# Performance work log

Hardware: AMD Instinct MI355X
Metric: run time of the kernel (lower is better)

Reference implementation:

```python
import jax, jax.numpy as jnp
import numpy as np

D_MODEL = 1024
NUM_HEADS = 16
D_K = D_MODEL // NUM_HEADS


def setup_inputs() -> dict:
    key = jax.random.key(0)
    ks = jax.random.split(key, 12)
    B, S, D = 4, 2048, D_MODEL
    s = 1.0 / np.sqrt(D)
    return {
        "q": jax.random.normal(ks[0], (B, S, D), jnp.float32),
        "k": jax.random.normal(ks[1], (B, S, D), jnp.float32),
        "v": jax.random.normal(ks[2], (B, S, D), jnp.float32),
        "w_q": jax.random.normal(ks[3], (D, D), jnp.float32) * s,
        "b_q": jax.random.normal(ks[4], (D,), jnp.float32) * s,
        "w_k": jax.random.normal(ks[5], (D, D), jnp.float32) * s,
        "b_k": jax.random.normal(ks[6], (D,), jnp.float32) * s,
        "w_v": jax.random.normal(ks[7], (D, D), jnp.float32) * s,
        "b_v": jax.random.normal(ks[8], (D,), jnp.float32) * s,
        "w_0": jax.random.normal(ks[9], (D, D), jnp.float32) * s,
        "b_0": jax.random.normal(ks[10], (D,), jnp.float32) * s,
    }


def reference(q, k, v, w_q, b_q, w_k, b_k, w_v, b_v, w_0, b_0):
    B = q.shape[0]
    H, dk = NUM_HEADS, D_K
    # project and split heads: [B,S,D] -> [B,H,S,dk]
    def split_heads(x):
        return x.reshape(B, -1, H, dk).transpose(0, 2, 1, 3)
    qh = split_heads(q @ w_q + b_q)
    kh = split_heads(k @ w_k + b_k)
    vh = split_heads(v @ w_v + b_v)
    scores = jnp.einsum("bhsd,bhtd->bhst", qh, kh) / np.sqrt(dk).astype(jnp.float32)
    dists = jax.nn.softmax(scores, axis=-1)
    attn = jnp.einsum("bhst,bhtd->bhsd", dists, vh)  # [B,H,S,dk]
    # NOTE: original torch code reshapes WITHOUT transposing heads back
    # (.contiguous().view(B, -1, d_model) on [B,H,S,dk]) -- reproduce faithfully.
    attn = attn.reshape(B, -1, D_MODEL)  # [B,S,D] with head-major interleave
    return attn @ w_0 + b_0
```

## Files before the change

kernel.cpp:

```cpp
#include <hip/hip_runtime.h>
#include <stdint.h>

typedef __bf16 bf16x8 __attribute__((ext_vector_type(8)));
typedef float  f32x4  __attribute__((ext_vector_type(4)));

union U16x8 { uint4 u; uint16_t s[8]; };

__device__ __forceinline__ uint16_t f2b(float f) {
    union { float f; uint32_t u; } c; c.f = f;
    uint32_t u = c.u;
    uint32_t r = u + 0x7fffu + ((u >> 16) & 1u);
    return (uint16_t)(r >> 16);
}

__device__ __forceinline__ uint32_t asu(float f) {
    union { float f; uint32_t u; } c; c.f = f; return c.u;
}
__device__ __forceinline__ uint32_t pack_bf16_hu(float a, float b) {
    uint32_t ua = asu(a) + 0x8000u, ub = asu(b) + 0x8000u;
    return (ua >> 16) | (ub & 0xffff0000u);
}

__device__ __forceinline__ void gl_lds16(const uint16_t* g, uint16_t* l) {
    __builtin_amdgcn_global_load_lds(
        (const __attribute__((address_space(1))) void*)g,
        (__attribute__((address_space(3))) void*)l, 16, 0, 0);
}

__global__ void cast3_f32_bf16(const float* __restrict__ x0, const float* __restrict__ x1,
                               const float* __restrict__ x2,
                               uint16_t* __restrict__ y0, uint16_t* __restrict__ y1,
                               uint16_t* __restrict__ y2, int n4) {
    const float* x; uint16_t* y;
    switch (blockIdx.y) {
        case 0: x = x0; y = y0; break;
        case 1: x = x1; y = y1; break;
        default: x = x2; y = y2; break;
    }
    int i = blockIdx.x * blockDim.x + threadIdx.x;
    if (i < n4) {
        float4 v = ((const float4*)x)[i];
        ushort4 o;
        o.x = f2b(v.x); o.y = f2b(v.y); o.z = f2b(v.z); o.w = f2b(v.w);
        *(ushort4*)(y + (size_t)i * 4) = o;
    }
}

__global__ void transpose_cast4(const float* __restrict__ W0, const float* __restrict__ W1,
                                const float* __restrict__ W2, const float* __restrict__ W3,
                                uint16_t* __restrict__ O0, uint16_t* __restrict__ O1,
                                uint16_t* __restrict__ O2, uint16_t* __restrict__ O3) {
    __shared__ float tile[64][65];
    const float* W; uint16_t* Wt;
    switch (blockIdx.z) {
        case 0: W = W0; Wt = O0; break;
        case 1: W = W1; Wt = O1; break;
        case 2: W = W2; Wt = O2; break;
        default: W = W3; Wt = O3; break;
    }
    const int k0 = blockIdx.y * 64, n0 = blockIdx.x * 64;
    const int tx = threadIdx.x & 63, ty = threadIdx.x >> 6;
    #pragma unroll
    for (int r = ty; r < 64; r += 4)
        tile[r][tx] = W[(size_t)(k0 + r) * 1024 + n0 + tx];
    __syncthreads();
    #pragma unroll
    for (int r = ty; r < 64; r += 4)
        Wt[(size_t)(n0 + r) * 1024 + k0 + tx] = f2b(tile[tx][r]);
}

__global__ __launch_bounds__(256, 3)
void gemm_qkv(const uint16_t* __restrict__ A0, const uint16_t* __restrict__ A1,
              const uint16_t* __restrict__ A2,
              const uint16_t* __restrict__ B0, const uint16_t* __restrict__ B1,
              const uint16_t* __restrict__ B2,
              const float* __restrict__ c0, const float* __restrict__ c1,
              const float* __restrict__ c2,
              uint16_t* __restrict__ O0, uint16_t* __restrict__ O1,
              uint16_t* __restrict__ O2, float qscale) {
    __shared__ uint16_t SH[2 * 128 * 32] __attribute__((aligned(16)));
    uint16_t* As = SH;
    uint16_t* Bs = SH + 128 * 32;

    const uint16_t* A; const uint16_t* Bt; const float* bias; uint16_t* Cout; float scale;
    switch (blockIdx.z) {
        case 0: A = A0; Bt = B0; bias = c0; Cout = O0; scale = qscale; break;
        case 1: A = A1; Bt = B1; bias = c1; Cout = O1; scale = 1.0f;  break;
        default: A = A2; Bt = B2; bias = c2; Cout = O2; scale = 1.0f; break;
    }

    const int tid = threadIdx.x;
    const int m0 = blockIdx.y * 128, n0 = blockIdx.x * 128;
    const int l = tid & 63, ln = l & 15, qd = l >> 4;
    const int w = tid >> 6;
    const int wm = (w >> 1) * 64, wn = (w & 1) * 64;

    f32x4 acc[4][4] = {};

    for (int kk = 0; kk < 1024; kk += 32) {
        __syncthreads();
        #pragma unroll
        for (int i = 0; i < 2; i++) {
            int c = tid + i * 256;
            gl_lds16(&A[(size_t)(m0 + (c >> 2)) * 1024 + kk + (c & 3) * 8], &As[c * 8]);
            gl_lds16(&Bt[(size_t)(n0 + (c >> 2)) * 1024 + kk + (c & 3) * 8], &Bs[c * 8]);
        }
        __syncthreads();

        bf16x8 af[4], bfr[4];
        #pragma unroll
        for (int i = 0; i < 4; i++)
            af[i] = *(const bf16x8*)&As[(wm + i * 16 + ln) * 32 + qd * 8];
        #pragma unroll
        for (int j = 0; j < 4; j++)
            bfr[j] = *(const bf16x8*)&Bs[(wn + j * 16 + ln) * 32 + qd * 8];
        #pragma unroll
        for (int i = 0; i < 4; i++)
            #pragma unroll
            for (int j = 0; j < 4; j++)
                acc[i][j] = __builtin_amdgcn_mfma_f32_16x16x32_bf16(af[i], bfr[j], acc[i][j], 0, 0, 0);
    }

    float bv[4];
    #pragma unroll
    for (int j = 0; j < 4; j++) bv[j] = bias[n0 + wn + j * 16 + ln];

    __syncthreads();
    uint16_t* scr = (uint16_t*)SH + w * 1024;
    const int colb = n0 + wn;
    const int h = colb >> 6;
    #pragma unroll
    for (int i = 0; i < 4; i++) {
        #pragma unroll
        for (int j = 0; j < 4; j++)
            #pragma unroll
            for (int r = 0; r < 4; r++)
                scr[(qd * 4 + r) * 64 + j * 16 + ln] = f2b((acc[i][j][r] + bv[j]) * scale);
        #pragma unroll
        for (int ii = 0; ii < 2; ii++) {
            int ch = ii * 64 + l, row = ch >> 3, sg = ch & 7;
            int grow = m0 + wm + i * 16 + row;
            int b = grow >> 11, s = grow & 2047;
            *(uint4*)&Cout[(size_t)((b * 16 + h) * 2048 + s) * 64 + sg * 8] =
                *(uint4*)&scr[row * 64 + sg * 8];
        }
    }
}

__global__ __launch_bounds__(256, 3)
void gemm_o(const uint16_t* __restrict__ A, const uint16_t* __restrict__ Bt,
            const float* __restrict__ bias, float* __restrict__ Cout) {
    __shared__ uint16_t SH[2 * 128 * 32] __attribute__((aligned(16)));
    uint16_t* As = SH;
    uint16_t* Bs = SH + 128 * 32;

    const int tid = threadIdx.x;
    const int m0 = blockIdx.y * 128, n0 = blockIdx.x * 128;
    const int l = tid & 63, ln = l & 15, qd = l >> 4;
    const int w = tid >> 6;
    const int wm = (w >> 1) * 64, wn = (w & 1) * 64;

    f32x4 acc[4][4] = {};

    for (int kk = 0; kk < 1024; kk += 32) {
        __syncthreads();
        #pragma unroll
        for (int i = 0; i < 2; i++) {
            int c = tid + i * 256;
            gl_lds16(&A[(size_t)(m0 + (c >> 2)) * 1024 + kk + (c & 3) * 8], &As[c * 8]);
            gl_lds16(&Bt[(size_t)(n0 + (c >> 2)) * 1024 + kk + (c & 3) * 8], &Bs[c * 8]);
        }
        __syncthreads();

        bf16x8 af[4], bfr[4];
        #pragma unroll
        for (int i = 0; i < 4; i++)
            af[i] = *(const bf16x8*)&As[(wm + i * 16 + ln) * 32 + qd * 8];
        #pragma unroll
        for (int j = 0; j < 4; j++)
            bfr[j] = *(const bf16x8*)&Bs[(wn + j * 16 + ln) * 32 + qd * 8];
        #pragma unroll
        for (int i = 0; i < 4; i++)
            #pragma unroll
            for (int j = 0; j < 4; j++)
                acc[i][j] = __builtin_amdgcn_mfma_f32_16x16x32_bf16(af[i], bfr[j], acc[i][j], 0, 0, 0);
    }

    float bv[4];
    #pragma unroll
    for (int j = 0; j < 4; j++) bv[j] = bias[n0 + wn + j * 16 + ln];

    __syncthreads();
    float* scr = (float*)SH + w * 1024;
    #pragma unroll
    for (int i = 0; i < 4; i++) {
        #pragma unroll
        for (int j = 0; j < 4; j++)
            #pragma unroll
            for (int r = 0; r < 4; r++)
                scr[(qd * 4 + r) * 64 + j * 16 + ln] = acc[i][j][r] + bv[j];
        #pragma unroll
        for (int ii = 0; ii < 4; ii++) {
            int ch = ii * 64 + l, row = ch >> 4, sg = ch & 15;
            *(float4*)&Cout[(size_t)(m0 + wm + i * 16 + row) * 1024 + n0 + wn + sg * 4] =
                *(float4*)&scr[row * 64 + sg * 4];
        }
    }
}

__global__ __launch_bounds__(512, 4)
void attn_kernel(const uint16_t* __restrict__ Qh, const uint16_t* __restrict__ Kh,
                 const uint16_t* __restrict__ Vh, uint16_t* __restrict__ Of) {
    __shared__ uint16_t Ks[64 * 72]  __attribute__((aligned(16)));
    __shared__ uint16_t Vt[64 * 72]  __attribute__((aligned(16)));
    __shared__ uint16_t Ps[256 * 72] __attribute__((aligned(16)));

    const int tid = threadIdx.x;
    const int w = tid >> 6, l = tid & 63, ln = l & 15, qd = l >> 4;
    const size_t base = (size_t)blockIdx.y * 131072;
    const int q0 = blockIdx.x * 256;

    bf16x8 qf[2][2];
    #pragma unroll
    for (int tq = 0; tq < 2; tq++)
        #pragma unroll
        for (int ks = 0; ks < 2; ks++)
            qf[tq][ks] = *(const bf16x8*)&Qh[base + (size_t)(q0 + w * 32 + tq * 16 + ln) * 64 + ks * 32 + qd * 8];

    f32x4 oacc[2][4] = {};
    float mrun[2] = { -__builtin_inff(), -__builtin_inff() };
    float lrun[2] = { 0.f, 0.f };

    for (int j = 0; j < 32; j++) {
        const int t0 = j * 64;
        __syncthreads();
        if (w >= 4) {
            int idx = tid - 256;
            #pragma unroll
            for (int i = 0; i < 2; i++) {
                int c = idx + i * 256, tr = c >> 3, sg = c & 7;
                *(uint4*)&Ks[tr * 72 + sg * 8] =
                    *(const uint4*)&Kh[base + (size_t)(t0 + tr) * 64 + sg * 8];
            }
        } else {
            int u = tid & 31, sg = tid >> 5;
            U16x8 r0, r1;
            r0.u = *(const uint4*)&Vh[base + (size_t)(t0 + 2 * u) * 64 + sg * 8];
            r1.u = *(const uint4*)&Vh[base + (size_t)(t0 + 2 * u + 1) * 64 + sg * 8];
            #pragma unroll
            for (int e = 0; e < 8; e++) {
                uint32_t pk = (uint32_t)r0.s[e] | ((uint32_t)r1.s[e] << 16);
                *(uint32_t*)&Vt[(sg * 8 + e) * 72 + 2 * u] = pk;
            }
        }
        __syncthreads();

        bf16x8 kb[4][2];
        #pragma unroll
        for (int tt = 0; tt < 4; tt++)
            #pragma unroll
            for (int ks = 0; ks < 2; ks++)
                kb[tt][ks] = *(const bf16x8*)&Ks[(tt * 16 + ln) * 72 + ks * 32 + qd * 8];
        f32x4 sa[4][2] = {};
        #pragma unroll
        for (int tt = 0; tt < 4; tt++)
            #pragma unroll
            for (int tq = 0; tq < 2; tq++)
                #pragma unroll
                for (int ks = 0; ks < 2; ks++)
                    sa[tt][tq] = __builtin_amdgcn_mfma_f32_16x16x32_bf16(kb[tt][ks], qf[tq][ks], sa[tt][tq], 0, 0, 0);

        float alpha[2];
        #pragma unroll
        for (int tq = 0; tq < 2; tq++) {
            float mx = -__builtin_inff();
            #pragma unroll
            for (int tt = 0; tt < 4; tt++)
                #pragma unroll
                for (int r = 0; r < 4; r++) mx = fmaxf(mx, sa[tt][tq][r]);
            mx = fmaxf(mx, __shfl_xor(mx, 16));
            mx = fmaxf(mx, __shfl_xor(mx, 32));
            float mnew = fmaxf(mrun[tq], mx);
            alpha[tq] = __builtin_amdgcn_exp2f(mrun[tq] - mnew);
            mrun[tq] = mnew;
            float rs = 0.f;
            #pragma unroll
            for (int tt = 0; tt < 4; tt++)
                #pragma unroll
                for (int r = 0; r < 4; r++) {
                    float p = __builtin_amdgcn_exp2f(sa[tt][tq][r] - mnew);
                    sa[tt][tq][r] = p; rs += p;
                }
            rs += __shfl_xor(rs, 16);
            rs += __shfl_xor(rs, 32);
            lrun[tq] = lrun[tq] * alpha[tq] + rs;
            #pragma unroll
            for (int tt = 0; tt < 4; tt++) {
                uint2 pk;
                pk.x = pack_bf16_hu(sa[tt][tq][0], sa[tt][tq][1]);
                pk.y = pack_bf16_hu(sa[tt][tq][2], sa[tt][tq][3]);
                *(uint2*)&Ps[(w * 32 + tq * 16 + ln) * 72 + tt * 16 + qd * 4] = pk;
            }
            #pragma unroll
            for (int dt = 0; dt < 4; dt++)
                #pragma unroll
                for (int r = 0; r < 4; r++) oacc[tq][dt][r] *= alpha[tq];
        }

        bf16x8 pa[2][2], vb[4][2];
        #pragma unroll
        for (int tq = 0; tq < 2; tq++)
            #pragma unroll
            for (int ks = 0; ks < 2; ks++)
                pa[tq][ks] = *(const bf16x8*)&Ps[(w * 32 + tq * 16 + ln) * 72 + ks * 32 + qd * 8];
        #pragma unroll
        for (int dt = 0; dt < 4; dt++)
            #pragma unroll
            for (int ks = 0; ks < 2; ks++)
                vb[dt][ks] = *(const bf16x8*)&Vt[(dt * 16 + ln) * 72 + ks * 32 + qd * 8];
        #pragma unroll
        for (int tq = 0; tq < 2; tq++)
            #pragma unroll
            for (int dt = 0; dt < 4; dt++)
                #pragma unroll
                for (int ks = 0; ks < 2; ks++)
                    oacc[tq][dt] = __builtin_amdgcn_mfma_f32_16x16x32_bf16(vb[dt][ks], pa[tq][ks], oacc[tq][dt], 0, 0, 0);
    }

    #pragma unroll
    for (int tq = 0; tq < 2; tq++) {
        float inv = 1.0f / lrun[tq];
        #pragma unroll
        for (int dt = 0; dt < 4; dt++) {
            uint2 pk;
            pk.x = pack_bf16_hu(oacc[tq][dt][0] * inv, oacc[tq][dt][1] * inv);
            pk.y = pack_bf16_hu(oacc[tq][dt][2] * inv, oacc[tq][dt][3] * inv);
            *(uint2*)&Ps[(w * 32 + tq * 16 + ln) * 72 + dt * 16 + qd * 4] = pk;
        }
    }
    __syncthreads();
    #pragma unroll
    for (int i = 0; i < 4; i++) {
        int c = tid + i * 512, row = c >> 3, sg = c & 7;
        *(uint4*)&Of[base + (size_t)(q0 + row) * 64 + sg * 8] =
            *(const uint4*)&Ps[row * 72 + sg * 8];
    }
}

extern "C" void kernel_launch(void* const* d_in, const int* in_sizes, int n_in,
                              void* d_out, int out_size, void* d_ws, size_t ws_size,
                              hipStream_t stream) {
    const float* q   = (const float*)d_in[0];
    const float* k   = (const float*)d_in[1];
    const float* v   = (const float*)d_in[2];
    const float* w_q = (const float*)d_in[3];
    const float* b_q = (const float*)d_in[4];
    const float* w_k = (const float*)d_in[5];
    const float* b_k = (const float*)d_in[6];
    const float* w_v = (const float*)d_in[7];
    const float* b_v = (const float*)d_in[8];
    const float* w_0 = (const float*)d_in[9];
    const float* b_0 = (const float*)d_in[10];

    uint16_t* ws  = (uint16_t*)d_ws;
    const size_t WE = 1048576, NE = 8388608;
    uint16_t* wtq = ws;
    uint16_t* wtk = wtq + WE;
    uint16_t* wtv = wtk + WE;
    uint16_t* wt0 = wtv + WE;
    uint16_t* xq  = wt0 + WE;
    uint16_t* xk  = xq + NE;
    uint16_t* xv  = xk + NE;
    uint16_t* Qh  = xv + NE;
    uint16_t* Kh  = Qh + NE;
    uint16_t* Vh  = Kh + NE;
    uint16_t* Pf  = xq;

    const dim3 tb(256);
    const dim3 gT(16, 16, 4);
    const dim3 gC(8192, 3);
    const dim3 gQ(8, 64, 3);
    const dim3 gO(8, 64);
    const dim3 gA(8, 64);
    const int  n4 = 2097152;

    const float qscale = 0.125f * 1.44269504f;

    transpose_cast4<<<gT, tb, 0, stream>>>(w_q, w_k, w_v, w_0, wtq, wtk, wtv, wt0);
    cast3_f32_bf16<<<gC, tb, 0, stream>>>(q, k, v, xq, xk, xv, n4);
    gemm_qkv<<<gQ, tb, 0, stream>>>(xq, xk, xv, wtq, wtk, wtv, b_q, b_k, b_v,
                                    Qh, Kh, Vh, qscale);
    attn_kernel<<<gA, dim3(512), 0, stream>>>(Qh, Kh, Vh, Pf);
    gemm_o<<<gO, tb, 0, stream>>>(Pf, wt0, b_0, (float*)d_out);
}
```

Baseline: 385.8 us.

## Double-buffer K/V tiles with async LDS loads, swizzle, lazy softmax rescale

Makes the K and V shared-memory tiles double-buffered. K for the next tile is prefetched with global_load_lds into an XOR-swizzled unpadded layout, and V is loaded into registers early and transposed into the other buffer after softmax. This drops one barrier per iteration and overlaps global loads with compute. It also skips the rescaling of the output accumulator when the row max grows by at most 8 (a lazy online-softmax threshold), and raises wave priority around the MFMA blocks. The risks are reliance on the buffer swap being ordered correctly by the single remaining barrier, higher register and LDS use, and exp2 overflow headroom with the lazy rescale.

```diff
diff --git a/kernel.cpp b/kernel.cpp
--- a/kernel.cpp
+++ b/kernel.cpp
@@ -211,15 +211,21 @@
 __global__ __launch_bounds__(512, 4)
 void attn_kernel(const uint16_t* __restrict__ Qh, const uint16_t* __restrict__ Kh,
                  const uint16_t* __restrict__ Vh, uint16_t* __restrict__ Of) {
-    __shared__ uint16_t Ks[64 * 72]  __attribute__((aligned(16)));
-    __shared__ uint16_t Vt[64 * 72]  __attribute__((aligned(16)));
-    __shared__ uint16_t Ps[256 * 72] __attribute__((aligned(16)));
+    __shared__ uint16_t Ks[2][64 * 64] __attribute__((aligned(16)));
+    __shared__ uint16_t Vt[2][64 * 72] __attribute__((aligned(16)));
+    __shared__ uint16_t Ps[256 * 72]   __attribute__((aligned(16)));
 
     const int tid = threadIdx.x;
     const int w = tid >> 6, l = tid & 63, ln = l & 15, qd = l >> 4;
     const size_t base = (size_t)blockIdx.y * 131072;
     const int q0 = blockIdx.x * 256;
 
+    const int krow = tid >> 3;
+    const int kchunk = (tid & 7) ^ (krow & 7);
+    const int swz0 = ((0 + qd) ^ (ln & 7)) * 8;
+    const int swz1 = ((4 + qd) ^ (ln & 7)) * 8;
+    const int vu = tid & 31, vsg = tid >> 5;
+
     bf16x8 qf[2][2];
     #pragma unroll
     for (int tq = 0; tq < 2; tq++)
@@ -231,37 +237,40 @@
     float mrun[2] = { -__builtin_inff(), -__builtin_inff() };
     float lrun[2] = { 0.f, 0.f };
 
+    gl_lds16(&Kh[base + (size_t)krow * 64 + kchunk * 8], &Ks[0][tid * 8]);
+    uint4 vr0, vr1;
+    if (w < 4) {
+        vr0 = *(const uint4*)&Vh[base + (size_t)(2 * vu) * 64 + vsg * 8];
+        vr1 = *(const uint4*)&Vh[base + (size_t)(2 * vu + 1) * 64 + vsg * 8];
+        U16x8 a, b; a.u = vr0; b.u = vr1;
+        #pragma unroll
+        for (int e = 0; e < 8; e++) {
+            uint32_t pk = (uint32_t)a.s[e] | ((uint32_t)b.s[e] << 16);
+            *(uint32_t*)&Vt[0][(vsg * 8 + e) * 72 + 2 * vu] = pk;
+        }
+    }
+
     for (int j = 0; j < 32; j++) {
-        const int t0 = j * 64;
+        const int cur = j & 1, nxt = cur ^ 1;
         __syncthreads();
-        if (w >= 4) {
-            int idx = tid - 256;
-            #pragma unroll
-            for (int i = 0; i < 2; i++) {
-                int c = idx + i * 256, tr = c >> 3, sg = c & 7;
-                *(uint4*)&Ks[tr * 72 + sg * 8] =
-                    *(const uint4*)&Kh[base + (size_t)(t0 + tr) * 64 + sg * 8];
+
+        if (j < 31) {
+            const int t0n = (j + 1) * 64;
+            gl_lds16(&Kh[base + (size_t)(t0n + krow) * 64 + kchunk * 8], &Ks[nxt][tid * 8]);
+            if (w < 4) {
+                vr0 = *(const uint4*)&Vh[base + (size_t)(t0n + 2 * vu) * 64 + vsg * 8];
+                vr1 = *(const uint4*)&Vh[base + (size_t)(t0n + 2 * vu + 1) * 64 + vsg * 8];
             }
-        } else {
-            int u = tid & 31, sg = tid >> 5;
-            U16x8 r0, r1;
-            r0.u = *(const uint4*)&Vh[base + (size_t)(t0 + 2 * u) * 64 + sg * 8];
-            r1.u = *(const uint4*)&Vh[base + (size_t)(t0 + 2 * u + 1) * 64 + sg * 8];
-            #pragma unroll
-            for (int e = 0; e < 8; e++) {
-                uint32_t pk = (uint32_t)r0.s[e] | ((uint32_t)r1.s[e] << 16);
-                *(uint32_t*)&Vt[(sg * 8 + e) * 72 + 2 * u] = pk;
-            }
-        }
-        __syncthreads();
+        }
 
         bf16x8 kb[4][2];
         #pragma unroll
-        for (int tt = 0; tt < 4; tt++)
-            #pragma unroll
-            for (int ks = 0; ks < 2; ks++)
-                kb[tt][ks] = *(const bf16x8*)&Ks[(tt * 16 + ln) * 72 + ks * 32 + qd * 8];
+        for (int tt = 0; tt < 4; tt++) {
+            kb[tt][0] = *(const bf16x8*)&Ks[cur][(tt * 16 + ln) * 64 + swz0];
+            kb[tt][1] = *(const bf16x8*)&Ks[cur][(tt * 16 + ln) * 64 + swz1];
+        }
         f32x4 sa[4][2] = {};
+        __builtin_amdgcn_s_setprio(1);
         #pragma unroll
         for (int tt = 0; tt < 4; tt++)
             #pragma unroll
@@ -269,8 +278,8 @@
                 #pragma unroll
                 for (int ks = 0; ks < 2; ks++)
                     sa[tt][tq] = __builtin_amdgcn_mfma_f32_16x16x32_bf16(kb[tt][ks], qf[tq][ks], sa[tt][tq], 0, 0, 0);
-
-        float alpha[2];
+        __builtin_amdgcn_s_setprio(0);
+
         #pragma unroll
         for (int tq = 0; tq < 2; tq++) {
             float mx = -__builtin_inff();
@@ -280,20 +289,39 @@
                 for (int r = 0; r < 4; r++) mx = fmaxf(mx, sa[tt][tq][r]);
             mx = fmaxf(mx, __shfl_xor(mx, 16));
             mx = fmaxf(mx, __shfl_xor(mx, 32));
-            float mnew = fmaxf(mrun[tq], mx);
-            alpha[tq] = __builtin_amdgcn_exp2f(mrun[tq] - mnew);
-            mrun[tq] = mnew;
-            float rs = 0.f;
-            #pragma unroll
-            for (int tt = 0; tt < 4; tt++)
-                #pragma unroll
-                for (int r = 0; r < 4; r++) {
-                    float p = __builtin_amdgcn_exp2f(sa[tt][tq][r] - mnew);
-                    sa[tt][tq][r] = p; rs += p;
-                }
-            rs += __shfl_xor(rs, 16);
-            rs += __shfl_xor(rs, 32);
-            lrun[tq] = lrun[tq] * alpha[tq] + rs;
+            if (__all(mx - mrun[tq] <= 8.0f)) {
+                const float m = mrun[tq];
+                float rs = 0.f;
+                #pragma unroll
+                for (int tt = 0; tt < 4; tt++)
+                    #pragma unroll
+                    for (int r = 0; r < 4; r++) {
+                        float p = __builtin_amdgcn_exp2f(sa[tt][tq][r] - m);
+                        sa[tt][tq][r] = p; rs += p;
+                    }
+                rs += __shfl_xor(rs, 16);
+                rs += __shfl_xor(rs, 32);
+                lrun[tq] += rs;
+            } else {
+                float mnew = fmaxf(mrun[tq], mx);
+                float al = __builtin_amdgcn_exp2f(mrun[tq] - mnew);
+                mrun[tq] = mnew;
+                float rs = 0.f;
+                #pragma unroll
+                for (int tt = 0; tt < 4; tt++)
+                    #pragma unroll
+                    for (int r = 0; r < 4; r++) {
+                        float p = __builtin_amdgcn_exp2f(sa[tt][tq][r] - mnew);
+                        sa[tt][tq][r] = p; rs += p;
+                    }
+                rs += __shfl_xor(rs, 16);
+                rs += __shfl_xor(rs, 32);
+                lrun[tq] = lrun[tq] * al + rs;
+                #pragma unroll
+                for (int dt = 0; dt < 4; dt++)
+                    #pragma unroll
+                    for (int r = 0; r < 4; r++) oacc[tq][dt][r] *= al;
+            }
             #pragma unroll
             for (int tt = 0; tt < 4; tt++) {
                 uint2 pk;
@@ -301,10 +329,15 @@
                 pk.y = pack_bf16_hu(sa[tt][tq][2], sa[tt][tq][3]);
                 *(uint2*)&Ps[(w * 32 + tq * 16 + ln) * 72 + tt * 16 + qd * 4] = pk;
             }
-            #pragma unroll
-            for (int dt = 0; dt < 4; dt++)
-                #pragma unroll
-                for (int r = 0; r < 4; r++) oacc[tq][dt][r] *= alpha[tq];
+        }
+
+        if (j < 31 && w < 4) {
+            U16x8 a, b; a.u = vr0; b.u = vr1;
+            #pragma unroll
+            for (int e = 0; e < 8; e++) {
+                uint32_t pk = (uint32_t)a.s[e] | ((uint32_t)b.s[e] << 16);
+                *(uint32_t*)&Vt[nxt][(vsg * 8 + e) * 72 + 2 * vu] = pk;
+            }
         }
 
         bf16x8 pa[2][2], vb[4][2];
@@ -317,7 +350,8 @@
         for (int dt = 0; dt < 4; dt++)
             #pragma unroll
             for (int ks = 0; ks < 2; ks++)
-                vb[dt][ks] = *(const bf16x8*)&Vt[(dt * 16 + ln) * 72 + ks * 32 + qd * 8];
+                vb[dt][ks] = *(const bf16x8*)&Vt[cur][(dt * 16 + ln) * 72 + ks * 32 + qd * 8];
+        __builtin_amdgcn_s_setprio(1);
         #pragma unroll
         for (int tq = 0; tq < 2; tq++)
             #pragma unroll
@@ -325,6 +359,7 @@
                 #pragma unroll
                 for (int ks = 0; ks < 2; ks++)
                     oacc[tq][dt] = __builtin_amdgcn_mfma_f32_16x16x32_bf16(vb[dt][ks], pa[tq][ks], oacc[tq][dt], 0, 0, 0);
+        __builtin_amdgcn_s_setprio(0);
     }
 
     #pragma unroll
```

Result: slower. 423.2 us (+9.7%).
